# Performance work log

Measured on AMD Instinct MI355X. Metric: run time of the kernel, lower is better.

Reference implementation:

```python
import jax, jax.numpy as jnp
import numpy as np

D_MODEL = 1024
N_HEADS = 16
D_KV = 64
INNER = N_HEADS * D_KV
NUM_BUCKETS = 32
MAX_DISTANCE = 128
B, S = 4, 2048


def _relative_position_bucket(relative_position):
    # Mirrors T5Attention._relative_position_bucket (bidirectional variant)
    num_buckets = NUM_BUCKETS // 2  # 16
    relative_buckets = (relative_position > 0).astype(jnp.int32) * num_buckets
    rp = jnp.abs(relative_position)
    max_exact = num_buckets // 2  # 8
    is_small = rp < max_exact
    # clamp to 1 before log to avoid -inf (masked out by where anyway)
    rp_large = max_exact + (
        jnp.log(jnp.maximum(rp, 1).astype(jnp.float32) / max_exact)
        / np.log(MAX_DISTANCE / max_exact)
        * (num_buckets - max_exact)
    ).astype(jnp.int32)
    rp_large = jnp.minimum(rp_large, num_buckets - 1)
    return relative_buckets + jnp.where(is_small, rp.astype(jnp.int32), rp_large)


def setup_inputs() -> dict:
    key = jax.random.key(0)
    k1, k2, k3, k4, k5, k6 = jax.random.split(key, 6)
    hidden_states = jax.random.normal(k1, (B, S, D_MODEL), dtype=jnp.float32)
    positions = jnp.arange(B * S, dtype=jnp.int64 if jax.config.jax_enable_x64 else jnp.int32).reshape(B, S)
    mask = jnp.ones((B, S), dtype=jnp.float32)
    sc = 1.0 / np.sqrt(D_MODEL)
    wq = jax.random.normal(k2, (INNER, D_MODEL), dtype=jnp.float32) * sc
    wk = jax.random.normal(k3, (INNER, D_MODEL), dtype=jnp.float32) * sc
    wv = jax.random.normal(k4, (INNER, D_MODEL), dtype=jnp.float32) * sc
    wo = jax.random.normal(k5, (D_MODEL, INNER), dtype=jnp.float32) * sc
    rel_bias = jax.random.normal(k6, (NUM_BUCKETS, N_HEADS), dtype=jnp.float32)
    return {"hidden_states": hidden_states, "positions": positions, "mask": mask,
            "wq": wq, "wk": wk, "wv": wv, "wo": wo, "rel_bias": rel_bias}


def reference(hidden_states, positions, mask, wq, wk, wv, wo, rel_bias):
    Bq, Sq, _ = hidden_states.shape

    def shape_heads(x):  # [B,S,inner] -> [B,H,S,dkv]
        return x.reshape(Bq, Sq, N_HEADS, D_KV).transpose(0, 2, 1, 3)

    # position bias: [B,H,Sq,Sk]
    rel_pos = positions[:, None, :] - positions[:, :, None]  # memory - context
    buckets = _relative_position_bucket(rel_pos)             # [B,Sq,Sk]
    position_bias = rel_bias[buckets].transpose(0, 3, 1, 2)  # [B,H,Sq,Sk]

    q = shape_heads(hidden_states @ wq.T).astype(jnp.float32)
    k = shape_heads(hidden_states @ wk.T).astype(jnp.float32)
    v = shape_heads(hidden_states @ wv.T).astype(jnp.float32)

    scores = jnp.einsum('bhqd,bhkd->bhqk', q, k)  # no 1/sqrt(d) scaling (T5)
    bias = position_bias - 1000.0 * (1.0 - mask[:, None, None, :])
    attn = jax.nn.softmax(scores + bias, axis=-1)  # dropout p=0

    ctx = jnp.einsum('bhqk,bhkd->bhqd', attn, v)
    ctx = ctx.transpose(0, 2, 1, 3).reshape(Bq, Sq, INNER).astype(hidden_states.dtype)
    return ctx @ wo.T
```

## Files before the change

kernel.cpp:

```cpp
#include <hip/hip_runtime.h>
#include <cstdint>
#include <cstddef>

#define D_MODEL 1024
#define N_HEADS 16
#define INNER   1024
#define NBATCH  4
#define SEQ     2048
#define MTOT    (NBATCH * SEQ)
#define LOG2E   1.44269504088896f
#define BSTRIDE 4352
#define MASKC   1442.695041f

typedef _Float16 f16;
typedef __attribute__((ext_vector_type(8))) _Float16 f16x8;
typedef __attribute__((ext_vector_type(4))) _Float16 f16x4;
typedef __attribute__((ext_vector_type(2))) _Float16 f16x2;
typedef __attribute__((ext_vector_type(2))) __fp16   h16x2;
typedef __attribute__((ext_vector_type(4))) float    f32x4;

__device__ __forceinline__ f16x2 cvtpk(float x, float y) {
#if __has_builtin(__builtin_amdgcn_cvt_pkrtz)
  h16x2 r = __builtin_amdgcn_cvt_pkrtz(x, y);
  return __builtin_bit_cast(f16x2, r);
#else
  f16x2 r; r[0] = (f16)x; r[1] = (f16)y; return r;
#endif
}
__device__ __forceinline__ float dot2acc(f16x2 p, float acc) {
#if __has_builtin(__builtin_amdgcn_fdot2)
  h16x2 a = __builtin_bit_cast(h16x2, p);
  h16x2 one; one[0] = (__fp16)1.0f; one[1] = (__fp16)1.0f;
  return __builtin_amdgcn_fdot2(a, one, acc, false);
#else
  return acc + (float)p[0] + (float)p[1];
#endif
}

__global__ void k_cvt(const float* __restrict__ src, f16* __restrict__ dst, int n4, float scale) {
  int i = blockIdx.x * 256 + threadIdx.x;
  if (i < n4) {
    const float4 v = reinterpret_cast<const float4*>(src)[i];
    f16x4 h;
    h[0] = (f16)(v.x * scale); h[1] = (f16)(v.y * scale);
    h[2] = (f16)(v.z * scale); h[3] = (f16)(v.w * scale);
    reinterpret_cast<f16x4*>(dst)[i] = h;
  }
}

__global__ void k_cvtw(const float* __restrict__ wq, const float* __restrict__ wk,
                       const float* __restrict__ wv, const float* __restrict__ wo,
                       f16* __restrict__ dq, f16* __restrict__ dk,
                       f16* __restrict__ dv, f16* __restrict__ dwo) {
  const int y = blockIdx.y;
  const float* src = y == 0 ? wq : (y == 1 ? wk : (y == 2 ? wv : wo));
  f16* dst = y == 0 ? dq : (y == 1 ? dk : (y == 2 ? dv : dwo));
  const float scale = y == 0 ? LOG2E : 1.0f;
  const int i = blockIdx.x * 256 + threadIdx.x;
  const float4 v = reinterpret_cast<const float4*>(src)[i];
  f16x4 h;
  h[0] = (f16)(v.x * scale); h[1] = (f16)(v.y * scale);
  h[2] = (f16)(v.z * scale); h[3] = (f16)(v.w * scale);
  reinterpret_cast<f16x4*>(dst)[i] = h;
}

__global__ void k_bias(const float* __restrict__ relb, float* __restrict__ biasG) {
  const int i = blockIdx.x * 256 + threadIdx.x;
  const int h = blockIdx.y;
  const int d = i - 2048;
  const int sgn = d > 0 ? 16 : 0;
  const int a = d < 0 ? -d : d;
  int bucket;
  if (a < 8) {
    bucket = a;
  } else {
    float t = logf((float)a / 8.0f);
    t = t / 2.772588722239781f;
    t = t * 8.0f;
    int lg = 8 + (int)t;
    bucket = lg < 15 ? lg : 15;
  }
  biasG[h * BSTRIDE + i] = relb[(sgn + bucket) * N_HEADS + h] * LOG2E - MASKC;
}

__device__ __forceinline__ void gload_lds16(const void* g, void* l) {
  __builtin_amdgcn_global_load_lds(
      (const __attribute__((address_space(1))) unsigned int*)g,
      (__attribute__((address_space(3))) unsigned int*)l,
      16, 0, 0);
}

template <int MODE>
__device__ __forceinline__ void gemm_body(const f16* __restrict__ A,
                                          const f16* __restrict__ W,
                                          void* __restrict__ Cp) {
  __shared__ __align__(16) f16 As[128 * 64];
  __shared__ __align__(16) f16 Bs[128 * 64];
  const int t = threadIdx.x;
  const int lane = t & 63;
  const int wid = t >> 6;
  const int wr = wid >> 1;
  const int wc = wid & 1;
  const int g = lane >> 4;
  const int lr = lane & 15;
  const int m0 = blockIdx.y * 128;
  const int n0 = blockIdx.x * 128;

  f32x4 acc[4][4] = {};
  const char* Ab = (const char*)A;
  const char* Wb = (const char*)W;

  for (int kt = 0; kt < D_MODEL / 64; ++kt) {
    const int k0 = kt * 64;
    __syncthreads();
#pragma unroll
    for (int i = 0; i < 4; ++i) {
      const int idx = i * 256 + t;
      const int row = idx >> 3;
      const int cb  = (idx & 7) * 16;
      gload_lds16(Ab + ((size_t)(m0 + row) * D_MODEL + k0) * 2 + cb, (char*)As + idx * 16);
      gload_lds16(Wb + ((size_t)(n0 + row) * D_MODEL + k0) * 2 + cb, (char*)Bs + idx * 16);
    }
    asm volatile("s_waitcnt vmcnt(0)" ::: "memory");
    __syncthreads();

    f16x8 af[4][2], bf[4][2];
#pragma unroll
    for (int mi = 0; mi < 4; ++mi)
#pragma unroll
      for (int kk = 0; kk < 2; ++kk)
        af[mi][kk] = *(const f16x8*)&As[(wr * 64 + mi * 16 + lr) * 64 + kk * 32 + g * 8];
#pragma unroll
    for (int ni = 0; ni < 4; ++ni)
#pragma unroll
      for (int kk = 0; kk < 2; ++kk)
        bf[ni][kk] = *(const f16x8*)&Bs[(wc * 64 + ni * 16 + lr) * 64 + kk * 32 + g * 8];
#pragma unroll
    for (int kk = 0; kk < 2; ++kk)
#pragma unroll
      for (int mi = 0; mi < 4; ++mi)
#pragma unroll
        for (int ni = 0; ni < 4; ++ni)
          acc[mi][ni] = __builtin_amdgcn_mfma_f32_16x16x32_f16(af[mi][kk], bf[ni][kk], acc[mi][ni], 0, 0, 0);
  }

#pragma unroll
  for (int mi = 0; mi < 4; ++mi)
#pragma unroll
    for (int ni = 0; ni < 4; ++ni) {
      const int n = n0 + wc * 64 + ni * 16 + lr;
      if (MODE == 2) {
        const int mbase = m0 + wr * 64 + mi * 16 + g * 4;
        const int b2 = mbase >> 11, s2 = mbase & (SEQ - 1);
        const int h2 = n >> 6, d2 = n & 63;
        const int sub = ((s2 & 15) >> 2) * 8 + ((s2 >> 4) & 1) * 4;
        f16x4 w;
#pragma unroll
        for (int r = 0; r < 4; ++r) w[r] = (f16)acc[mi][ni][r];
        *(f16x4*)((f16*)Cp + ((size_t)((b2 * 16 + h2) * 64 + d2) * SEQ + (s2 >> 5) * 32 + sub)) = w;
      } else {
#pragma unroll
        for (int r = 0; r < 4; ++r) {
          const int m = m0 + wr * 64 + mi * 16 + g * 4 + r;
          if (MODE == 1)
            ((float*)Cp)[(size_t)m * INNER + n] = acc[mi][ni][r];
          else
            ((f16*)Cp)[(size_t)m * INNER + n] = (f16)acc[mi][ni][r];
        }
      }
    }
}

__global__ __launch_bounds__(256) void k_gemm_qkv(
    const f16* __restrict__ A,
    const f16* __restrict__ Wq, const f16* __restrict__ Wk, const f16* __restrict__ Wv,
    f16* __restrict__ Cq, f16* __restrict__ Ck, f16* __restrict__ Vt) {
  if (blockIdx.z == 0)      gemm_body<0>(A, Wq, Cq);
  else if (blockIdx.z == 1) gemm_body<0>(A, Wk, Ck);
  else                      gemm_body<2>(A, Wv, Vt);
}

__global__ __launch_bounds__(256) void k_gemm_out(
    const f16* __restrict__ A, const f16* __restrict__ W, float* __restrict__ C) {
  gemm_body<1>(A, W, C);
}

__global__ __launch_bounds__(256, 4) void k_attn(
    const f16* __restrict__ Q, const f16* __restrict__ K, const f16* __restrict__ Vt,
    const float* __restrict__ biasG, const float* __restrict__ mask,
    f16* __restrict__ ctx) {
  __shared__ __align__(16) float biasT[2176];
  __shared__ __align__(16) f16 Ks[2 * 2048];
  __shared__ __align__(16) f16 Vs[2 * 2048];

  const int nb = (int)blockIdx.x;
  const int v = (nb & 7) * 128 + (nb >> 3);
  const int bh = v >> 4, qc = v & 15;
  const int b = bh >> 4, h = bh & 15;

  const int t = threadIdx.x, lane = t & 63, wid = t >> 6;
  const int g = lane >> 4, lr = lane & 15;
  const int qb = qc * 128;

  {
    const float* bgh = biasG + (size_t)h * BSTRIDE + (1921 - qb);
    for (int i = t; i < 2176; i += 256) biasT[i] = bgh[i];
  }

  const char* Kg = (const char*)K + ((size_t)(b * SEQ) * INNER + h * 64) * 2;
  const char* Vg = (const char*)Vt + ((size_t)bh * 64) * SEQ * 2;
  const float* maskB = mask + (size_t)b * SEQ;
  const int krow = t >> 3, kch = t & 7;
  const int ksrc = (kch * 16) ^ ((krow & 7) << 4);
  const int vrow = t >> 2, vch = t & 3;
  const int vsrc = (vch * 16) ^ ((vrow & 3) << 4);

  const int qw = qb + wid * 32;

  f16x8 qa[2][2];
#pragma unroll
  for (int hh = 0; hh < 2; ++hh)
#pragma unroll
    for (int kk = 0; kk < 2; ++kk)
      qa[hh][kk] = *(const f16x8*)&Q[(size_t)(b * SEQ + qw + hh * 16 + lr) * INNER + h * 64 + kk * 32 + g * 8];

  int koffs[2][2], voffs[4];
#pragma unroll
  for (int s = 0; s < 2; ++s)
#pragma unroll
    for (int hf = 0; hf < 2; ++hf)
      koffs[s][hf] = (s * 16 + lr) * 128 + ((hf * 64 + g * 16) ^ ((lr & 7) << 4));
#pragma unroll
  for (int dn = 0; dn < 4; ++dn)
    voffs[dn] = (dn * 16 + lr) * 64 + ((g * 16) ^ ((lr & 3) << 4));

  f32x4 o[2][4] = {};
  float mrun[2] = {-__builtin_inff(), -__builtin_inff()};
  float lsum[2] = {0.0f, 0.0f};
  const int jbase = 127 + 4 * g - wid * 32 - lr;

  gload_lds16(Kg + ((size_t)krow * INNER) * 2 + ksrc, (char*)Ks + t * 16);
  gload_lds16(Vg + ((size_t)vrow * SEQ) * 2 + vsrc,   (char*)Vs + t * 16);
  asm volatile("s_waitcnt vmcnt(0)" ::: "memory");
  __syncthreads();

#define ATTN_ITER(BUF, K0)                                                     \
  {                                                                            \
    const float4 mk0 = *(const float4*)(maskB + (K0) + 4 * g);                 \
    const float4 mk1 = *(const float4*)(maskB + (K0) + 16 + 4 * g);            \
    const int k0n_ = ((K0) + 32 < SEQ) ? (K0) + 32 : 0;                        \
    gload_lds16(Kg + ((size_t)(k0n_ + krow) * INNER) * 2 + ksrc,               \
                (char*)Ks + ((BUF) ^ 1) * 4096 + t * 16);                      \
    gload_lds16(Vg + ((size_t)vrow * SEQ + k0n_) * 2 + vsrc,                   \
                (char*)Vs + ((BUF) ^ 1) * 4096 + t * 16);                      \
    f16x8 kf[2][2];                                                            \
    _Pragma("unroll") for (int s = 0; s < 2; ++s)                              \
      _Pragma("unroll") for (int hf = 0; hf < 2; ++hf)                         \
        kf[s][hf] = *(const f16x8*)((const char*)Ks + (BUF) * 4096 + koffs[s][hf]); \
    f16x8 vv[4];                                                               \
    _Pragma("unroll") for (int dn = 0; dn < 4; ++dn)                           \
      vv[dn] = *(const f16x8*)((const char*)Vs + (BUF) * 4096 + voffs[dn]);    \
    f32x4 sg[2][2];                                                            \
    _Pragma("unroll") for (int hh = 0; hh < 2; ++hh)                           \
      _Pragma("unroll") for (int s = 0; s < 2; ++s) {                          \
        const int jA = (K0) + s * 16 + jbase - hh * 16;                        \
        const float* mkp = (s == 0) ? (const float*)&mk0 : (const float*)&mk1; \
        f32x4 z;                                                               \
        _Pragma("unroll") for (int r = 0; r < 4; ++r)                          \
          z[r] = fmaf(mkp[r], MASKC, biasT[jA + r]);                           \
        z = __builtin_amdgcn_mfma_f32_16x16x32_f16(kf[s][0], qa[hh][0], z, 0, 0, 0); \
        z = __builtin_amdgcn_mfma_f32_16x16x32_f16(kf[s][1], qa[hh][1], z, 0, 0, 0); \
        sg[hh][s] = z;                                                         \
      }                                                                        \
    float mxA = fmaxf(fmaxf(fmaxf(sg[0][0][0], sg[0][0][1]), fmaxf(sg[0][0][2], sg[0][0][3])), \
                      fmaxf(fmaxf(sg[0][1][0], sg[0][1][1]), fmaxf(sg[0][1][2], sg[0][1][3]))); \
    float mxB = fmaxf(fmaxf(fmaxf(sg[1][0][0], sg[1][0][1]), fmaxf(sg[1][0][2], sg[1][0][3])), \
                      fmaxf(fmaxf(sg[1][1][0], sg[1][1][1]), fmaxf(sg[1][1][2], sg[1][1][3]))); \
    if (__any((mxA > mrun[0] + 11.5415603f) || (mxB > mrun[1] + 11.5415603f))) { \
      mxA = fmaxf(mxA, __shfl_xor(mxA, 16));                                   \
      mxB = fmaxf(mxB, __shfl_xor(mxB, 16));                                   \
      mxA = fmaxf(mxA, __shfl_xor(mxA, 32));                                   \
      mxB = fmaxf(mxB, __shfl_xor(mxB, 32));                                   \
      const float mnA = fmaxf(mrun[0], mxA), mnB = fmaxf(mrun[1], mxB);        \
      const float aA = __builtin_amdgcn_exp2f(mrun[0] - mnA);                  \
      const float aB = __builtin_amdgcn_exp2f(mrun[1] - mnB);                  \
      lsum[0] *= aA; lsum[1] *= aB;                                            \
      _Pragma("unroll") for (int dn = 0; dn < 4; ++dn)                         \
        _Pragma("unroll") for (int r = 0; r < 4; ++r) {                        \
          o[0][dn][r] *= aA; o[1][dn][r] *= aB;                                \
        }                                                                      \
      mrun[0] = mnA; mrun[1] = mnB;                                            \
    }                                                                          \
    f16x4 pfA[2], pfB[2];                                                      \
    _Pragma("unroll") for (int s = 0; s < 2; ++s) {                            \
      float eA[4], eB[4];                                                      \
      _Pragma("unroll") for (int r = 0; r < 4; ++r) {                          \
        eA[r] = __builtin_amdgcn_exp2f(sg[0][s][r] - mrun[0]);                 \
        eB[r] = __builtin_amdgcn_exp2f(sg[1][s][r] - mrun[1]);                 \
      }                                                                        \
      const f16x2 a0 = cvtpk(eA[0], eA[1]), a1 = cvtpk(eA[2], eA[3]);          \
      const f16x2 b0 = cvtpk(eB[0], eB[1]), b1 = cvtpk(eB[2], eB[3]);          \
      lsum[0] = dot2acc(a0, lsum[0]); lsum[0] = dot2acc(a1, lsum[0]);          \
      lsum[1] = dot2acc(b0, lsum[1]); lsum[1] = dot2acc(b1, lsum[1]);          \
      pfA[s][0] = a0[0]; pfA[s][1] = a0[1]; pfA[s][2] = a1[0]; pfA[s][3] = a1[1]; \
      pfB[s][0] = b0[0]; pfB[s][1] = b0[1]; pfB[s][2] = b1[0]; pfB[s][3] = b1[1]; \
    }                                                                          \
    _Pragma("unroll") for (int dn = 0; dn < 4; ++dn) {                         \
      const f16x4 v0 = __builtin_shufflevector(vv[dn], vv[dn], 0, 1, 2, 3);    \
      const f16x4 v1 = __builtin_shufflevector(vv[dn], vv[dn], 4, 5, 6, 7);    \
      o[0][dn] = __builtin_amdgcn_mfma_f32_16x16x16f16(v0, pfA[0], o[0][dn], 0, 0, 0); \
      o[0][dn] = __builtin_amdgcn_mfma_f32_16x16x16f16(v1, pfA[1], o[0][dn], 0, 0, 0); \
      o[1][dn] = __builtin_amdgcn_mfma_f32_16x16x16f16(v0, pfB[0], o[1][dn], 0, 0, 0); \
      o[1][dn] = __builtin_amdgcn_mfma_f32_16x16x16f16(v1, pfB[1], o[1][dn], 0, 0, 0); \
    }                                                                          \
    asm volatile("s_waitcnt vmcnt(0)" ::: "memory");                           \
    __syncthreads();                                                           \
  }

  for (int k0 = 0; k0 < SEQ; k0 += 64) {
    ATTN_ITER(0, k0)
    ATTN_ITER(1, k0 + 32)
  }

  lsum[0] += __shfl_xor(lsum[0], 16);
  lsum[1] += __shfl_xor(lsum[1], 16);
  lsum[0] += __shfl_xor(lsum[0], 32);
  lsum[1] += __shfl_xor(lsum[1], 32);

  const float invA = 1.0f / lsum[0], invB = 1.0f / lsum[1];
#pragma unroll
  for (int dn = 0; dn < 4; ++dn) {
    f16x4 wA, wB;
#pragma unroll
    for (int r = 0; r < 4; ++r) {
      wA[r] = (f16)(o[0][dn][r] * invA);
      wB[r] = (f16)(o[1][dn][r] * invB);
    }
    *(f16x4*)&ctx[(size_t)(b * SEQ + qw + lr) * INNER + h * 64 + dn * 16 + 4 * g] = wA;
    *(f16x4*)&ctx[(size_t)(b * SEQ + qw + 16 + lr) * INNER + h * 64 + dn * 16 + 4 * g] = wB;
  }
}

extern "C" void kernel_launch(void* const* d_in, const int* in_sizes, int n_in,
                              void* d_out, int out_size, void* d_ws, size_t ws_size,
                              hipStream_t stream) {
  const float* hs   = (const float*)d_in[0];
  const float* mask = (const float*)d_in[2];
  const float* wq   = (const float*)d_in[3];
  const float* wk   = (const float*)d_in[4];
  const float* wv   = (const float*)d_in[5];
  const float* wo   = (const float*)d_in[6];
  const float* relb = (const float*)d_in[7];

  char* ws = (char*)d_ws;
  const size_t SZ16 = (size_t)MTOT * INNER * 2;
  const size_t WSZ  = (size_t)INNER * D_MODEL * 2;
  f16* hs16 = (f16*)(ws);
  f16* q16  = (f16*)(ws + SZ16);
  f16* k16  = (f16*)(ws + 2 * SZ16);
  f16* vt16 = (f16*)(ws + 3 * SZ16);
  f16* wq16 = (f16*)(ws + 4 * SZ16);
  f16* wk16 = (f16*)(ws + 4 * SZ16 + WSZ);
  f16* wv16 = (f16*)(ws + 4 * SZ16 + 2 * WSZ);
  f16* wo16 = (f16*)(ws + 4 * SZ16 + 3 * WSZ);
  float* biasG = (float*)(ws + 4 * SZ16 + 4 * WSZ);

  k_cvt<<<(MTOT * INNER / 4 + 255) / 256, 256, 0, stream>>>(hs, hs16, MTOT * INNER / 4, 1.0f);
  k_cvtw<<<dim3(INNER * D_MODEL / 4 / 256, 4), 256, 0, stream>>>(
      wq, wk, wv, wo, wq16, wk16, wv16, wo16);

  k_bias<<<dim3(BSTRIDE / 256, N_HEADS), 256, 0, stream>>>(relb, biasG);

  k_gemm_qkv<<<dim3(INNER / 128, MTOT / 128, 3), 256, 0, stream>>>(
      hs16, wq16, wk16, wv16, q16, k16, vt16);

  k_attn<<<dim3(1024), 256, 0, stream>>>(
      q16, k16, vt16, biasG, mask, hs16);

  k_gemm_out<<<dim3(D_MODEL / 128, MTOT / 128), 256, 0, stream>>>(
      hs16, wo16, (float*)d_out);
}
```

Measured before the change: 244.9 us.

## Swizzle GEMM block order per XCD and vectorize attention bias loads

Both GEMM kernels move to a 1D grid and remap block IDs so that the blocks landing on each XCD (bid & 7) cover a contiguous band of M rows, which is meant to improve L2 reuse of A and W tiles. In attention, a second copy of the bias row shifted by one element is kept in LDS so that the per-lane bias fetches become aligned float2 loads whatever the parity of the lane offset. The six loaded pairs are shared across the hh/s combinations, replacing the sixteen scalar LDS reads per iteration. This costs extra LDS (about 8.7KB per block), which may lower attention occupancy.

```diff
diff --git a/kernel.cpp b/kernel.cpp
--- a/kernel.cpp
+++ b/kernel.cpp
@@ -93,7 +93,8 @@
 template <int MODE>
 __device__ __forceinline__ void gemm_body(const f16* __restrict__ A,
                                           const f16* __restrict__ W,
-                                          void* __restrict__ Cp) {
+                                          void* __restrict__ Cp,
+                                          int m0, int n0) {
   __shared__ __align__(16) f16 As[128 * 64];
   __shared__ __align__(16) f16 Bs[128 * 64];
   const int t = threadIdx.x;
@@ -103,8 +104,6 @@
   const int wc = wid & 1;
   const int g = lane >> 4;
   const int lr = lane & 15;
-  const int m0 = blockIdx.y * 128;
-  const int n0 = blockIdx.x * 128;
 
   f32x4 acc[4][4] = {};
   const char* Ab = (const char*)A;
@@ -175,21 +174,30 @@
     const f16* __restrict__ A,
     const f16* __restrict__ Wq, const f16* __restrict__ Wk, const f16* __restrict__ Wv,
     f16* __restrict__ Cq, f16* __restrict__ Ck, f16* __restrict__ Vt) {
-  if (blockIdx.z == 0)      gemm_body<0>(A, Wq, Cq);
-  else if (blockIdx.z == 1) gemm_body<0>(A, Wk, Ck);
-  else                      gemm_body<2>(A, Wv, Vt);
+  const int bid = (int)blockIdx.x;
+  const int X = bid & 7, l = bid >> 3;
+  const int zy = X * 24 + (l >> 3);
+  const int x = l & 7;
+  const int z = zy >> 6, y = zy & 63;
+  if (z == 0)      gemm_body<0>(A, Wq, Cq, y * 128, x * 128);
+  else if (z == 1) gemm_body<0>(A, Wk, Ck, y * 128, x * 128);
+  else             gemm_body<2>(A, Wv, Vt, y * 128, x * 128);
 }
 
 __global__ __launch_bounds__(256) void k_gemm_out(
     const f16* __restrict__ A, const f16* __restrict__ W, float* __restrict__ C) {
-  gemm_body<1>(A, W, C);
+  const int bid = (int)blockIdx.x;
+  const int X = bid & 7, l = bid >> 3;
+  const int y = X * 8 + (l >> 3), x = l & 7;
+  gemm_body<1>(A, W, C, y * 128, x * 128);
 }
 
 __global__ __launch_bounds__(256, 4) void k_attn(
     const f16* __restrict__ Q, const f16* __restrict__ K, const f16* __restrict__ Vt,
     const float* __restrict__ biasG, const float* __restrict__ mask,
     f16* __restrict__ ctx) {
-  __shared__ __align__(16) float biasT[2176];
+  __shared__ __align__(16) float  biasT[2178];
+  __shared__ __align__(16) float2 biasO[1088];
   __shared__ __align__(16) f16 Ks[2 * 2048];
   __shared__ __align__(16) f16 Vs[2 * 2048];
 
@@ -204,7 +212,11 @@
 
   {
     const float* bgh = biasG + (size_t)h * BSTRIDE + (1921 - qb);
-    for (int i = t; i < 2176; i += 256) biasT[i] = bgh[i];
+    for (int i = t; i < 2177; i += 256) biasT[i] = bgh[i];
+    for (int m = t; m < 1088; m += 256) {
+      float2 o2; o2.x = bgh[2 * m + 1]; o2.y = bgh[2 * m + 2];
+      biasO[m] = o2;
+    }
   }
 
   const char* Kg = (const char*)K + ((size_t)(b * SEQ) * INNER + h * 64) * 2;
@@ -237,7 +249,11 @@
   f32x4 o[2][4] = {};
   float mrun[2] = {-__builtin_inff(), -__builtin_inff()};
   float lsum[2] = {0.0f, 0.0f};
+
   const int jbase = 127 + 4 * g - wid * 32 - lr;
+  const int jb2 = jbase - 16;
+  const char* biasPtr = (jb2 & 1) ? ((const char*)biasO + (size_t)(jb2 - 1) * 4)
+                                  : ((const char*)biasT + (size_t)jb2 * 4);
 
   gload_lds16(Kg + ((size_t)krow * INNER) * 2 + ksrc, (char*)Ks + t * 16);
   gload_lds16(Vg + ((size_t)vrow * SEQ) * 2 + vsrc,   (char*)Vs + t * 16);
@@ -253,6 +269,16 @@
                 (char*)Ks + ((BUF) ^ 1) * 4096 + t * 16);                      \
     gload_lds16(Vg + ((size_t)vrow * SEQ + k0n_) * 2 + vsrc,                   \
                 (char*)Vs + ((BUF) ^ 1) * 4096 + t * 16);                      \
+    const char* bb = biasPtr + (K0) * 4;                                       \
+    const float2 bm0 = *(const float2*)(bb);                                   \
+    const float2 bm1 = *(const float2*)(bb + 8);                               \
+    const float2 bc0 = *(const float2*)(bb + 64);                              \
+    const float2 bc1 = *(const float2*)(bb + 72);                              \
+    const float2 bp0 = *(const float2*)(bb + 128);                             \
+    const float2 bp1 = *(const float2*)(bb + 136);                             \
+    const float bsel[2][2][4] = {                                              \
+        {{bc0.x, bc0.y, bc1.x, bc1.y}, {bp0.x, bp0.y, bp1.x, bp1.y}},          \
+        {{bm0.x, bm0.y, bm1.x, bm1.y}, {bc0.x, bc0.y, bc1.x, bc1.y}}};         \
     f16x8 kf[2][2];                                                            \
     _Pragma("unroll") for (int s = 0; s < 2; ++s)                              \
       _Pragma("unroll") for (int hf = 0; hf < 2; ++hf)                         \
@@ -263,11 +289,10 @@
     f32x4 sg[2][2];                                                            \
     _Pragma("unroll") for (int hh = 0; hh < 2; ++hh)                           \
       _Pragma("unroll") for (int s = 0; s < 2; ++s) {                          \
-        const int jA = (K0) + s * 16 + jbase - hh * 16;                        \
         const float* mkp = (s == 0) ? (const float*)&mk0 : (const float*)&mk1; \
         f32x4 z;                                                               \
         _Pragma("unroll") for (int r = 0; r < 4; ++r)                          \
-          z[r] = fmaf(mkp[r], MASKC, biasT[jA + r]);                           \
+          z[r] = fmaf(mkp[r], MASKC, bsel[hh][s][r]);                          \
         z = __builtin_amdgcn_mfma_f32_16x16x32_f16(kf[s][0], qa[hh][0], z, 0, 0, 0); \
         z = __builtin_amdgcn_mfma_f32_16x16x32_f16(kf[s][1], qa[hh][1], z, 0, 0, 0); \
         sg[hh][s] = z;                                                         \
@@ -371,12 +396,12 @@
 
   k_bias<<<dim3(BSTRIDE / 256, N_HEADS), 256, 0, stream>>>(relb, biasG);
 
-  k_gemm_qkv<<<dim3(INNER / 128, MTOT / 128, 3), 256, 0, stream>>>(
+  k_gemm_qkv<<<dim3(1536), 256, 0, stream>>>(
       hs16, wq16, wk16, wv16, q16, k16, vt16);
 
   k_attn<<<dim3(1024), 256, 0, stream>>>(
       q16, k16, vt16, biasG, mask, hs16);
 
-  k_gemm_out<<<dim3(D_MODEL / 128, MTOT / 128), 256, 0, stream>>>(
+  k_gemm_out<<<dim3(512), 256, 0, stream>>>(
       hs16, wo16, (float*)d_out);
 }
```

Measured after the change: 240.6 us. About the same (-1.8%).
